# Kernel tuning notes

Hardware: AMD Instinct MI355X
Metric: run time of the kernel (lower is better)

## Reference

```python
import jax, jax.numpy as jnp
import numpy as np
import math

B, N, DIM, H, DH, NNULL = 2, 2048, 1024, 16, 64, 2
SCALE = 8.0
LN_EPS = 1e-5


def _alibi_slopes(heads):
    # heads is a power of 2 here (16): slopes = start * start**i
    start = 2.0 ** (-(2.0 ** (-(math.log2(heads) - 3))))
    return np.array([start * (start ** i) for i in range(heads)], dtype=np.float32)


def setup_inputs() -> dict:
    key = jax.random.key(0)
    ks = jax.random.split(key, 6)
    inner = H * DH
    return {
        "x": jax.random.normal(ks[0], (B, N, DIM), dtype=jnp.float32),
        "norm_g": jnp.ones((DIM,), jnp.float32),
        "norm_b": jnp.zeros((DIM,), jnp.float32),
        "Wq": jax.random.normal(ks[1], (DIM, inner), jnp.float32) * 0.02,
        "Wkv": jax.random.normal(ks[2], (DIM, 2 * inner), jnp.float32) * 0.02,
        "q_scale": jnp.ones((DH,), jnp.float32),
        "k_scale": jnp.ones((DH,), jnp.float32),
        "null_kv": jax.random.normal(ks[3], (H, 2 * NNULL, DH), jnp.float32),
        "Wout": jax.random.normal(ks[4], (inner, DIM), jnp.float32) * 0.02,
    }


def _l2norm(t):
    # matches F.normalize: x / max(||x||, 1e-12)
    n = jnp.sqrt(jnp.sum(t * t, axis=-1, keepdims=True))
    return t / jnp.maximum(n, 1e-12)


def reference(x, norm_g, norm_b, Wq, Wkv, q_scale, k_scale, null_kv, Wout):
    b, n, dim = x.shape
    h, dh, nn = H, DH, NNULL
    j = n + nn

    # NOTE: faithful to source -- K/V come from the PRE-norm x (kv_input bound
    # before x = self.norm(x)); only Q uses the LayerNorm'd x.
    mu = jnp.mean(x, axis=-1, keepdims=True)
    var = jnp.mean((x - mu) ** 2, axis=-1, keepdims=True)
    xn = (x - mu) * jax.lax.rsqrt(var + LN_EPS) * norm_g + norm_b

    q = (xn @ Wq).reshape(b, n, h, dh).transpose(0, 2, 1, 3)          # b h n d
    kv = x @ Wkv
    k, v = jnp.split(kv, 2, axis=-1)
    k = k.reshape(b, n, h, dh).transpose(0, 2, 1, 3)                   # b h n d
    v = v.reshape(b, n, h, dh).transpose(0, 2, 1, 3)

    # null kv: (h, 2*nn, dh) -> (h, nn, 2, dh)
    null = null_kv.reshape(h, nn, 2, dh)
    nk = jnp.broadcast_to(null[:, :, 0, :][None], (b, h, nn, dh))
    nv = jnp.broadcast_to(null[:, :, 1, :][None], (b, h, nn, dh))
    k = jnp.concatenate([nk, k], axis=2)                               # b h j d
    v = jnp.concatenate([nv, v], axis=2)

    q = _l2norm(q) * q_scale
    k = _l2norm(k) * k_scale

    sim = jnp.einsum('bhid,bhjd->bhij', q, k) * SCALE                  # b h n j

    # ALiBi bias: rows at positions j-n..j-1, cols 0..j-1
    irow = jnp.arange(j - n, j)
    jcol = jnp.arange(j)
    bias = -jnp.abs(jcol[None, :] - irow[:, None]).astype(sim.dtype)   # (n, j)
    slopes = jnp.asarray(_alibi_slopes(h))[:, None, None]              # (h,1,1)
    sim = sim + slopes * bias

    # causal mask: triu with offset j - n + 1 (null kv always visible)
    causal = jnp.triu(jnp.ones((n, j), dtype=bool), k=j - n + 1)
    neg = jnp.finfo(sim.dtype).max
    sim = jnp.where(causal[None, None], -neg, sim)

    attn = jax.nn.softmax(sim, axis=-1)
    out = jnp.einsum('bhij,bhjd->bhid', attn, v)
    out = out.transpose(0, 2, 1, 3).reshape(b, n, h * dh)
    return out @ Wout
```

## Files before the change

kernel.cpp:

```cpp
#include <hip/hip_runtime.h>
#include <hip/hip_bf16.h>
#include <stdint.h>

#define H_    16
#define N_    2048
#define DIM_  1024
#define DH_   64
#define NN_   2
#define J_    2050
#define JP_   2112
#define B_    2
#define M_    4096
#define NSEG_ 84

#define S8L_  11.541560327111707f
#define LOG2E_ 1.4426950408889634f

typedef unsigned short u16;
typedef unsigned int u32;
typedef short bf16x8 __attribute__((ext_vector_type(8)));
typedef float f32x4 __attribute__((ext_vector_type(4)));

__device__ __forceinline__ u16 f2b(float f) {
  union { float f; unsigned int i; } v; v.f = f;
  unsigned int r = v.i + 0x7fffu + ((v.i >> 16) & 1u);
  return (u16)(r >> 16);
}
__device__ __forceinline__ float lo2f(u32 u) {
  union { u32 i; float f; } v; v.i = u << 16; return v.f;
}
__device__ __forceinline__ float hi2f(u32 u) {
  union { u32 i; float f; } v; v.i = u & 0xffff0000u; return v.f;
}
__device__ __forceinline__ void unp8(const uint4 u, float* d) {
  d[0] = lo2f(u.x); d[1] = hi2f(u.x); d[2] = lo2f(u.y); d[3] = hi2f(u.y);
  d[4] = lo2f(u.z); d[5] = hi2f(u.z); d[6] = lo2f(u.w); d[7] = hi2f(u.w);
}
__device__ __forceinline__ u32 pk2(float a, float b) {
  union { __hip_bfloat162 h; u32 u; } x;
  x.h = __float22bfloat162_rn(make_float2(a, b));
  return x.u;
}
__device__ __forceinline__ void dma16(const u16* g, u16* l) {
  __builtin_amdgcn_global_load_lds(
      (const __attribute__((address_space(1))) u32*)(const void*)g,
      (__attribute__((address_space(3))) u32*)(void*)l, 16, 0, 0);
}

__global__ __launch_bounds__(256) void prep_k(const float* __restrict__ x,
                                              const float* __restrict__ g,
                                              const float* __restrict__ bb,
                                              const float* __restrict__ Wq,
                                              const float* __restrict__ Wkv,
                                              const float* __restrict__ Wout,
                                              const float* __restrict__ nkv,
                                              const float* __restrict__ ks,
                                              u16* __restrict__ xn,
                                              u16* __restrict__ xbf,
                                              u16* __restrict__ WqT,
                                              u16* __restrict__ WkvT,
                                              u16* __restrict__ WoutT,
                                              u16* __restrict__ Kb,
                                              u16* __restrict__ VTp) {
  __shared__ float tile[32][33];
  __shared__ float red[8];
  int bx = blockIdx.x, by = blockIdx.y;
  int t = threadIdx.x;
  if (bx < 128) {
    const float* in; u16* out; int C; int cx;
    if (bx < 32)      { in = Wq;   out = WqT;   C = 1024; cx = bx; }
    else if (bx < 96) { in = Wkv;  out = WkvT;  C = 2048; cx = bx - 32; }
    else              { in = Wout; out = WoutT; C = 1024; cx = bx - 96; }
    const int R = 1024;
    int tx = t & 31, ty = t >> 5;
    int c0 = cx * 32, r0 = by * 32;
    #pragma unroll
    for (int i = 0; i < 32; i += 8)
      tile[ty + i][tx] = in[(size_t)(r0 + ty + i) * C + c0 + tx];
    __syncthreads();
    #pragma unroll
    for (int i = 0; i < 32; i += 8)
      out[(size_t)(c0 + ty + i) * R + r0 + tx] = f2b(tile[tx][ty + i]);
  } else if (bx < 256) {
    int row = (bx - 128) * 32 + by;
    float4 rw = *(const float4*)(x + (size_t)row * DIM_ + t * 4);
    float v0 = rw.x, v1 = rw.y, v2 = rw.z, v3 = rw.w;
    uint2 cw;
    cw.x = pk2(v0, v1);
    cw.y = pk2(v2, v3);
    *(uint2*)(xbf + (size_t)row * DIM_ + t * 4) = cw;
    float s = v0 + v1 + v2 + v3;
    float ss = v0 * v0 + v1 * v1 + v2 * v2 + v3 * v3;
    #pragma unroll
    for (int o = 32; o; o >>= 1) { s += __shfl_xor(s, o, 64); ss += __shfl_xor(ss, o, 64); }
    int lane = t & 63, w = t >> 6;
    if (lane == 0) { red[w] = s; red[4 + w] = ss; }
    __syncthreads();
    float S = red[0] + red[1] + red[2] + red[3];
    float SS = red[4] + red[5] + red[6] + red[7];
    float mu = S * (1.0f / DIM_);
    float var = SS * (1.0f / DIM_) - mu * mu;
    float rs = rsqrtf(var + 1e-5f);
    float4 gv = *(const float4*)(g + t * 4);
    float4 bv = *(const float4*)(bb + t * 4);
    uint2 ow;
    ow.x = pk2((v0 - mu) * rs * gv.x + bv.x, (v1 - mu) * rs * gv.y + bv.y);
    ow.y = pk2((v2 - mu) * rs * gv.z + bv.z, (v3 - mu) * rs * gv.w + bv.w);
    *(uint2*)(xn + (size_t)row * DIM_ + t * 4) = ow;
  } else if (bx == 256) {
    int bh = by, h = bh & 15;
    if (t < 128) {
      int j = t >> 6, d = t & 63;
      float kv = nkv[(size_t)(h * 4 + 2 * j) * 64 + d];
      float vv = nkv[(size_t)(h * 4 + 2 * j + 1) * 64 + d];
      float ssp = kv * kv;
      #pragma unroll
      for (int o = 32; o; o >>= 1) ssp += __shfl_xor(ssp, o, 64);
      float inv = 1.0f / fmaxf(sqrtf(ssp), 1e-12f);
      Kb[((size_t)bh * JP_ + j) * 64 + d] = f2b(kv * inv * ks[d]);
      VTp[((size_t)bh * 64 + d) * JP_ + j] = f2b(vv);
    }
  } else if (bx == 257) {
    int bh = by;
    uint4 z = {0, 0, 0, 0};
    u16* dst = Kb + ((size_t)bh * JP_ + 2048) * 64 + t * 16;
    ((uint4*)dst)[0] = z;
    ((uint4*)dst)[1] = z;
  } else {
    int bh = by;
    uint4 z = {0, 0, 0, 0};
    int d = t >> 2, p0 = (t & 3) * 16;
    u16* dst = VTp + ((size_t)bh * 64 + d) * JP_ + 2048 + p0;
    ((uint4*)dst)[0] = z;
    ((uint4*)dst)[1] = z;
  }
}

template <int MODE>
__global__ __launch_bounds__(256) void gemm_k(const u16* __restrict__ A,
                                              const u16* __restrict__ BT,
                                              void* __restrict__ dst0,
                                              void* __restrict__ dst1,
                                              const float* __restrict__ scale,
                                              int M, int Nc, int K) {
  __shared__ u16 As[2][128 * 64];
  __shared__ u16 Bs[2][128 * 64];
  int tid = threadIdx.x, wv = tid >> 6, lane = tid & 63;
  int fm = lane & 15, fg = lane >> 4;
  int fg4 = fg * 4;
  int wr = wv >> 1, wc = wv & 1;
  int nlin = (int)blockIdx.x + (int)gridDim.x * (int)blockIdx.y;
  int gx = (int)gridDim.x;
  int ypc = (int)gridDim.y >> 3;
  int mm = nlin >> 3;
  int row0 = ((nlin & 7) * ypc + mm / gx) * 128;
  int col0 = (mm % gx) * 128;
  f32x4 acc[4][4] = {};
  int srow = lane >> 3;
  int skb = ((lane & 7) ^ srow) * 8;
  const u16* Ag = A + (size_t)(row0 + wv * 32 + srow) * K + skb;
  const u16* Bg = BT + (size_t)(col0 + wv * 32 + srow) * K + skb;
  int fr7 = fm & 7;
  int ak0 = (fg ^ fr7) * 8;
  int ak1 = ((fg + 4) ^ fr7) * 8;
  auto stageg = [&](int k0, int buf) {
    u16* AsW = As[buf] + (wv * 32) * 64;
    u16* BsW = Bs[buf] + (wv * 32) * 64;
    dma16(Ag + k0,                    AsW);
    dma16(Ag + (size_t)8 * K + k0,    AsW + 8 * 64);
    dma16(Ag + (size_t)16 * K + k0,   AsW + 16 * 64);
    dma16(Ag + (size_t)24 * K + k0,   AsW + 24 * 64);
    dma16(Bg + k0,                    BsW);
    dma16(Bg + (size_t)8 * K + k0,    BsW + 8 * 64);
    dma16(Bg + (size_t)16 * K + k0,   BsW + 16 * 64);
    dma16(Bg + (size_t)24 * K + k0,   BsW + 24 * 64);
  };
  stageg(0, 0);
  __syncthreads();
  int cur = 0;
  for (int k0 = 0; k0 < K; k0 += 64) {
    if (k0 + 64 < K) stageg(k0 + 64, cur ^ 1);
    bf16x8 af0[4], af1[4], bf0[4], bf1[4];
    #pragma unroll
    for (int mt = 0; mt < 4; mt++) {
      int rbase = (wr * 64 + mt * 16 + fm) * 64;
      af0[mt] = *(const bf16x8*)&As[cur][rbase + ak0];
      af1[mt] = *(const bf16x8*)&As[cur][rbase + ak1];
    }
    #pragma unroll
    for (int nt = 0; nt < 4; nt++) {
      int rbase = (wc * 64 + nt * 16 + fm) * 64;
      bf0[nt] = *(const bf16x8*)&Bs[cur][rbase + ak0];
      bf1[nt] = *(const bf16x8*)&Bs[cur][rbase + ak1];
    }
    #pragma unroll
    for (int mt = 0; mt < 4; mt++)
      #pragma unroll
      for (int nt = 0; nt < 4; nt++) {
        acc[mt][nt] = __builtin_amdgcn_mfma_f32_16x16x32_bf16(af0[mt], bf0[nt], acc[mt][nt], 0, 0, 0);
        acc[mt][nt] = __builtin_amdgcn_mfma_f32_16x16x32_bf16(af1[mt], bf1[nt], acc[mt][nt], 0, 0, 0);
      }
    __syncthreads();
    cur ^= 1;
  }
  int colw = col0 + wc * 64;
  if (MODE == 1) {
    float* C = (float*)dst0;
    #pragma unroll
    for (int mt = 0; mt < 4; mt++)
      #pragma unroll
      for (int r = 0; r < 4; r++) {
        int m = row0 + wr * 64 + mt * 16 + fg4 + r;
        #pragma unroll
        for (int nt = 0; nt < 4; nt++)
          C[(size_t)m * Nc + colw + nt * 16 + fm] = acc[mt][nt][r];
      }
  } else {
    bool isK = (MODE == 2) || (colw < 1024);
    int h = (isK ? colw : colw - 1024) >> 6;
    if (isK) {
      float sv[4];
      #pragma unroll
      for (int nt = 0; nt < 4; nt++) sv[nt] = scale[nt * 16 + fm];
      if (MODE == 2) {
        #pragma unroll
        for (int nt = 0; nt < 4; nt++) sv[nt] *= S8L_;
      }
      u16* Do = (u16*)dst0;
      #pragma unroll
      for (int mt = 0; mt < 4; mt++) {
        #pragma unroll
        for (int r = 0; r < 4; r++) {
          float ssp = 0.0f;
          #pragma unroll
          for (int nt = 0; nt < 4; nt++) ssp += acc[mt][nt][r] * acc[mt][nt][r];
          #pragma unroll
          for (int o = 1; o <= 8; o <<= 1) ssp += __shfl_xor(ssp, o, 64);
          float inv = 1.0f / fmaxf(sqrtf(ssp), 1e-12f);
          int m = row0 + wr * 64 + mt * 16 + fg4 + r;
          int b = m >> 11, n = m & 2047;
          size_t base;
          if (MODE == 2) base = (((size_t)(b * H_ + h)) * N_ + n) * 64;
          else           base = (((size_t)(b * H_ + h)) * JP_ + (n + NN_)) * 64;
          #pragma unroll
          for (int nt = 0; nt < 4; nt++)
            Do[base + nt * 16 + fm] = f2b(acc[mt][nt][r] * inv * sv[nt]);
        }
      }
    } else {
      u16* Do = (u16*)dst1;
      #pragma unroll
      for (int mt = 0; mt < 4; mt++) {
        #pragma unroll
        for (int r = 0; r < 4; r++) {
          int m = row0 + wr * 64 + mt * 16 + fg4 + r;
          int b = m >> 11, n = m & 2047;
          int j = n + NN_;
          int c2 = j >> 6, jl = j & 63;
          int rem = jl & 31;
          int pos = (jl >> 5) * 32 + ((rem >> 2) & 3) * 8 + (rem >> 4) * 4 + (rem & 3);
          size_t hb = (size_t)(b * H_ + h) * 64;
          int off = c2 * 64 + pos;
          #pragma unroll
          for (int nt = 0; nt < 4; nt++)
            Do[(hb + nt * 16 + fm) * JP_ + off] = f2b(acc[mt][nt][r]);
        }
      }
    }
  }
}

__global__ __launch_bounds__(256, 6) void attn_k(const u16* __restrict__ Qn,
                                                 const u16* __restrict__ Kb,
                                                 const u16* __restrict__ VTp,
                                                 const float* __restrict__ qs,
                                                 const float* __restrict__ ks,
                                                 u16* __restrict__ partials) {
  __shared__ u16 Ks0[64 * 32], Ks1[64 * 32];
  __shared__ u16 Vs0[64 * 32], Vs1[64 * 32];
  int tid = threadIdx.x;
  int wv = tid >> 6, lane = tid & 63;
  int fm = lane & 15, fg = lane >> 4;
  int n = (int)blockIdx.x + NSEG_ * (int)blockIdx.y;
  int m = n >> 3;
  int bh = (n & 7) * 4 + m / NSEG_;
  int segid = m % NSEG_;
  int h = bh & 15;
  int cum = 0, qt = 0, seg = 0;
  #pragma unroll 1
  for (int i = 0; i < 32; i++) {
    int t = 31 - i, s = (t + 9) >> 3;
    if (segid < cum + s) { qt = t; seg = segid - cum; break; }
    cum += s;
  }
  int q0 = qt * 64;
  int q = q0 + wv * 16 + fm;
  float slope = exp2f(-0.5f * (float)(h + 1));
  float prod = fabsf(qs[lane] * ks[lane]);
  #pragma unroll
  for (int o = 32; o; o >>= 1) prod = fmaxf(prod, __shfl_xor(prod, o, 64));
  float MbL = 8.0f * prod * LOG2E_;
  float slopeL = slope * LOG2E_;
  const u16* qp = Qn + ((size_t)bh * N_ + q) * 64 + fg * 8;
  bf16x8 qf0 = *(const bf16x8*)(qp);
  bf16x8 qf1 = *(const bf16x8*)(qp + 32);
  f32x4 accO[4] = {};
  float lp = 0.0f;
  int lr = lane >> 2;
  int kbs = ((lane & 3) ^ ((lane >> 3) & 3)) * 8;
  int fs = (fg ^ ((fm >> 1) & 3)) * 8;
  const u16* KbBH = Kb + (size_t)bh * JP_ * 64;
  const u16* VTbh = VTp + (size_t)bh * 64 * JP_;
  int c0 = seg * 8;
  int c1 = min(c0 + 8, qt + 2);
  float bias0 = slopeL * (float)(c0 * 64 + fg * 4 - q - 2) - MbL;
  float sr1 = slopeL, sr2 = slopeL * 2.0f, sr3 = slopeL * 3.0f;
  float s16 = slopeL * 16.0f;
  float d64 = slopeL * 64.0f;
  for (int c = c0; c < c1; c++) {
    int jb = c * 64;
    __syncthreads();
    const u16* Kg = KbBH + (size_t)(jb + wv * 16 + lr) * 64 + kbs;
    dma16(Kg,      Ks0 + wv * 512);
    dma16(Kg + 32, Ks1 + wv * 512);
    const u16* Vg = VTbh + (size_t)(wv * 16 + lr) * JP_ + jb + kbs;
    dma16(Vg,      Vs0 + wv * 512);
    dma16(Vg + 32, Vs1 + wv * 512);
    __syncthreads();
    f32x4 accS[4] = {};
    #pragma unroll
    for (int nt = 0; nt < 4; nt++) {
      bf16x8 kf0 = *(const bf16x8*)&Ks0[(nt * 16 + fm) * 32 + fs];
      accS[nt] = __builtin_amdgcn_mfma_f32_16x16x32_bf16(kf0, qf0, accS[nt], 0, 0, 0);
      bf16x8 kf1 = *(const bf16x8*)&Ks1[(nt * 16 + fm) * 32 + fs];
      accS[nt] = __builtin_amdgcn_mfma_f32_16x16x32_bf16(kf1, qf1, accS[nt], 0, 0, 0);
    }
    union { bf16x8 v; u32 u[4]; } P0, P1;
    float lps = 0.0f;
    float bnt = bias0;
    if (c < qt) {
      #pragma unroll
      for (int nt = 0; nt < 4; nt++) {
        float e0 = __builtin_amdgcn_exp2f(accS[nt][0] + bnt);
        float e1 = __builtin_amdgcn_exp2f((accS[nt][1] + sr1) + bnt);
        float e2 = __builtin_amdgcn_exp2f((accS[nt][2] + sr2) + bnt);
        float e3 = __builtin_amdgcn_exp2f((accS[nt][3] + sr3) + bnt);
        u32 w0 = pk2(e0, e1);
        u32 w1 = pk2(e2, e3);
        lps += (e0 + e1) + (e2 + e3);
        if (nt < 2) { P0.u[nt * 2] = w0; P0.u[nt * 2 + 1] = w1; }
        else        { P1.u[(nt - 2) * 2] = w0; P1.u[(nt - 2) * 2 + 1] = w1; }
        bnt += s16;
      }
    } else {
      int thr = q + 2 - jb;
      #pragma unroll
      for (int nt = 0; nt < 4; nt++) {
        int ib = nt * 16 + fg * 4;
        float e0 = __builtin_amdgcn_exp2f(accS[nt][0] + bnt);
        float e1 = __builtin_amdgcn_exp2f((accS[nt][1] + sr1) + bnt);
        float e2 = __builtin_amdgcn_exp2f((accS[nt][2] + sr2) + bnt);
        float e3 = __builtin_amdgcn_exp2f((accS[nt][3] + sr3) + bnt);
        e0 = (ib + 0 <= thr) ? e0 : 0.0f;
        e1 = (ib + 1 <= thr) ? e1 : 0.0f;
        e2 = (ib + 2 <= thr) ? e2 : 0.0f;
        e3 = (ib + 3 <= thr) ? e3 : 0.0f;
        u32 w0 = pk2(e0, e1);
        u32 w1 = pk2(e2, e3);
        lps += (e0 + e1) + (e2 + e3);
        if (nt < 2) { P0.u[nt * 2] = w0; P0.u[nt * 2 + 1] = w1; }
        else        { P1.u[(nt - 2) * 2] = w0; P1.u[(nt - 2) * 2 + 1] = w1; }
        bnt += s16;
      }
    }
    lp += lps;
    bias0 += d64;
    #pragma unroll
    for (int nt = 0; nt < 4; nt++) {
      bf16x8 vf0 = *(const bf16x8*)&Vs0[(nt * 16 + fm) * 32 + fs];
      accO[nt] = __builtin_amdgcn_mfma_f32_16x16x32_bf16(vf0, P0.v, accO[nt], 0, 0, 0);
      bf16x8 vf1 = *(const bf16x8*)&Vs1[(nt * 16 + fm) * 32 + fs];
      accO[nt] = __builtin_amdgcn_mfma_f32_16x16x32_bf16(vf1, P1.v, accO[nt], 0, 0, 0);
    }
  }
  lp += __shfl_xor(lp, 16, 64);
  lp += __shfl_xor(lp, 32, 64);
  u16* P = partials + ((size_t)bh * NSEG_ + segid) * 4224;
  int sq = wv * 16 + fm;
  #pragma unroll
  for (int nt = 0; nt < 4; nt++) {
    uint2 ow;
    ow.x = pk2(accO[nt][0], accO[nt][1]);
    ow.y = pk2(accO[nt][2], accO[nt][3]);
    *(uint2*)(P + sq * 64 + nt * 16 + fg * 4) = ow;
  }
  if (fg == 0) *(float*)(P + 4096 + 2 * sq) = lp;
}

__global__ __launch_bounds__(256) void comb_k(const u16* __restrict__ partials,
                                              u16* __restrict__ AO) {
  int qt = blockIdx.x, bh = blockIdx.y, b = bh >> 4, h = bh & 15;
  int t = threadIdx.x, q = t >> 2, dq = (t & 3) * 16;
  int s = (qt + 9) >> 3;
  int cum = 0;
  for (int tt = qt + 1; tt < 32; tt++) cum += (tt + 9) >> 3;
  float acc[16] = {};
  float lsum = 0.0f;
  for (int k = 0; k < s; k++) {
    const u16* P = partials + ((size_t)bh * NSEG_ + cum + k) * 4224;
    uint4 a = *(const uint4*)(P + q * 64 + dq);
    uint4 bq = *(const uint4*)(P + q * 64 + dq + 8);
    float tmp[8];
    unp8(a, tmp);
    #pragma unroll
    for (int e = 0; e < 8; e++) acc[e] += tmp[e];
    unp8(bq, tmp);
    #pragma unroll
    for (int e = 0; e < 8; e++) acc[8 + e] += tmp[e];
    lsum += *(const float*)(P + 4096 + 2 * q);
  }
  float linv = 1.0f / lsum;
  int n = qt * 64 + q;
  u16* dst = AO + (((size_t)(b * N_ + n)) * H_ + h) * 64 + dq;
  u16 ov[16] __attribute__((aligned(16)));
  #pragma unroll
  for (int e = 0; e < 16; e++) ov[e] = f2b(acc[e] * linv);
  *(uint4*)dst = ((uint4*)ov)[0];
  *(uint4*)(dst + 8) = ((uint4*)ov)[1];
}

extern "C" void kernel_launch(void* const* d_in, const int* in_sizes, int n_in,
                              void* d_out, int out_size, void* d_ws, size_t ws_size,
                              hipStream_t stream) {
  const float* x    = (const float*)d_in[0];
  const float* ng   = (const float*)d_in[1];
  const float* nb   = (const float*)d_in[2];
  const float* Wq   = (const float*)d_in[3];
  const float* Wkv  = (const float*)d_in[4];
  const float* qs   = (const float*)d_in[5];
  const float* ks   = (const float*)d_in[6];
  const float* nkv  = (const float*)d_in[7];
  const float* Wout = (const float*)d_in[8];
  float* out = (float*)d_out;
  char* ws = (char*)d_ws;

  u16* xn    = (u16*)(ws + 0);
  u16* WoutT = (u16*)(ws + 8388608);
  u16* Qn    = (u16*)(ws + 10485760);
  u16* Kb    = (u16*)(ws + 18874368);
  u16* VTp   = (u16*)(ws + 27525120);
  u16* xbf   = (u16*)(ws + 36175872);
  u16* WqT   = (u16*)(ws + 44564480);
  u16* WkvT  = (u16*)(ws + 46661632);
  u16* parts = xbf;
  u16* AO    = xn;

  prep_k<<<dim3(259, 32), 256, 0, stream>>>(x, ng, nb, Wq, Wkv, Wout, nkv, ks,
                                            xn, xbf, WqT, WkvT, WoutT, Kb, VTp);
  gemm_k<2><<<dim3(8, 32), 256, 0, stream>>>(xn, WqT, Qn, nullptr, qs, M_, 1024, 1024);
  gemm_k<3><<<dim3(16, 32), 256, 0, stream>>>(xbf, WkvT, Kb, VTp, ks, M_, 2048, 1024);
  attn_k<<<dim3(NSEG_, 32), 256, 0, stream>>>(Qn, Kb, VTp, qs, ks, parts);
  comb_k<<<dim3(32, 32), 256, 0, stream>>>(parts, AO);
  gemm_k<1><<<dim3(8, 32), 256, 0, stream>>>(AO, WoutT, out, nullptr, nullptr, M_, 1024, 1024);
}
```

Measured before the change: 211.5 us.

## Merge Q and KV projection GEMMs into one launch and double-buffer K in attention

The Q and KV projection GEMMs now run as a single 768-block launch that branches on block index, removing one kernel launch and the tail between the two GEMMs. In the attention kernel, K tiles are double-buffered: the next K tile is prefetched while the current one is used, and explicit vmcnt waits with split barriers replace the two full __syncthreads per iteration. This is meant to hide K load latency behind compute. In exchange, the attention kernel uses more LDS, and the prefetch on the last iteration reads one K tile past c1, which relies on the padded buffer staying in bounds.

```diff
diff --git a/kernel.cpp b/kernel.cpp
--- a/kernel.cpp
+++ b/kernel.cpp
@@ -136,24 +136,31 @@
   }
 }
 
-template <int MODE>
-__global__ __launch_bounds__(256) void gemm_k(const u16* __restrict__ A,
-                                              const u16* __restrict__ BT,
-                                              void* __restrict__ dst0,
-                                              void* __restrict__ dst1,
-                                              const float* __restrict__ scale,
-                                              int M, int Nc, int K) {
+__global__ __launch_bounds__(256) void gemmqkv_k(const u16* __restrict__ xn,
+                                                 const u16* __restrict__ WqT,
+                                                 const u16* __restrict__ xbf,
+                                                 const u16* __restrict__ WkvT,
+                                                 u16* __restrict__ Qn,
+                                                 u16* __restrict__ Kb,
+                                                 u16* __restrict__ VTp,
+                                                 const float* __restrict__ qs,
+                                                 const float* __restrict__ ks) {
   __shared__ u16 As[2][128 * 64];
   __shared__ u16 Bs[2][128 * 64];
+  const int K = 1024;
   int tid = threadIdx.x, wv = tid >> 6, lane = tid & 63;
   int fm = lane & 15, fg = lane >> 4;
   int fg4 = fg * 4;
   int wr = wv >> 1, wc = wv & 1;
-  int nlin = (int)blockIdx.x + (int)gridDim.x * (int)blockIdx.y;
-  int gx = (int)gridDim.x;
-  int ypc = (int)gridDim.y >> 3;
-  int mm = nlin >> 3;
-  int row0 = ((nlin & 7) * ypc + mm / gx) * 128;
+  int nlin = (int)blockIdx.x;
+  bool isQ = nlin < 256;
+  const u16* A;
+  const u16* BT;
+  int gx, local;
+  if (isQ) { A = xn;  BT = WqT;  gx = 8;  local = nlin; }
+  else     { A = xbf; BT = WkvT; gx = 16; local = nlin - 256; }
+  int mm = local >> 3;
+  int row0 = ((local & 7) * 4 + mm / gx) * 128;
   int col0 = (mm % gx) * 128;
   f32x4 acc[4][4] = {};
   int srow = lane >> 3;
@@ -204,70 +211,132 @@
     cur ^= 1;
   }
   int colw = col0 + wc * 64;
-  if (MODE == 1) {
-    float* C = (float*)dst0;
-    #pragma unroll
-    for (int mt = 0; mt < 4; mt++)
+  bool isK = isQ || (colw < 1024);
+  int h = (isK ? colw : colw - 1024) >> 6;
+  if (isK) {
+    const float* scale = isQ ? qs : ks;
+    float sv[4];
+    #pragma unroll
+    for (int nt = 0; nt < 4; nt++) sv[nt] = scale[nt * 16 + fm];
+    if (isQ) {
+      #pragma unroll
+      for (int nt = 0; nt < 4; nt++) sv[nt] *= S8L_;
+    }
+    u16* Do = isQ ? Qn : Kb;
+    #pragma unroll
+    for (int mt = 0; mt < 4; mt++) {
+      #pragma unroll
+      for (int r = 0; r < 4; r++) {
+        float ssp = 0.0f;
+        #pragma unroll
+        for (int nt = 0; nt < 4; nt++) ssp += acc[mt][nt][r] * acc[mt][nt][r];
+        #pragma unroll
+        for (int o = 1; o <= 8; o <<= 1) ssp += __shfl_xor(ssp, o, 64);
+        float inv = 1.0f / fmaxf(sqrtf(ssp), 1e-12f);
+        int m = row0 + wr * 64 + mt * 16 + fg4 + r;
+        int b = m >> 11, n = m & 2047;
+        size_t base;
+        if (isQ) base = (((size_t)(b * H_ + h)) * N_ + n) * 64;
+        else     base = (((size_t)(b * H_ + h)) * JP_ + (n + NN_)) * 64;
+        #pragma unroll
+        for (int nt = 0; nt < 4; nt++)
+          Do[base + nt * 16 + fm] = f2b(acc[mt][nt][r] * inv * sv[nt]);
+      }
+    }
+  } else {
+    #pragma unroll
+    for (int mt = 0; mt < 4; mt++) {
       #pragma unroll
       for (int r = 0; r < 4; r++) {
         int m = row0 + wr * 64 + mt * 16 + fg4 + r;
+        int b = m >> 11, n = m & 2047;
+        int j = n + NN_;
+        int c2 = j >> 6, jl = j & 63;
+        int rem = jl & 31;
+        int pos = (jl >> 5) * 32 + ((rem >> 2) & 3) * 8 + (rem >> 4) * 4 + (rem & 3);
+        size_t hb = (size_t)(b * H_ + h) * 64;
+        int off = c2 * 64 + pos;
         #pragma unroll
         for (int nt = 0; nt < 4; nt++)
-          C[(size_t)m * Nc + colw + nt * 16 + fm] = acc[mt][nt][r];
+          VTp[(hb + nt * 16 + fm) * JP_ + off] = f2b(acc[mt][nt][r]);
       }
-  } else {
-    bool isK = (MODE == 2) || (colw < 1024);
-    int h = (isK ? colw : colw - 1024) >> 6;
-    if (isK) {
-      float sv[4];
-      #pragma unroll
-      for (int nt = 0; nt < 4; nt++) sv[nt] = scale[nt * 16 + fm];
-      if (MODE == 2) {
-        #pragma unroll
-        for (int nt = 0; nt < 4; nt++) sv[nt] *= S8L_;
+    }
+  }
+}
+
+__global__ __launch_bounds__(256) void gemm1_k(const u16* __restrict__ A,
+                                               const u16* __restrict__ BT,
+                                               float* __restrict__ C,
+                                               int M, int Nc, int K) {
+  __shared__ u16 As[2][128 * 64];
+  __shared__ u16 Bs[2][128 * 64];
+  int tid = threadIdx.x, wv = tid >> 6, lane = tid & 63;
+  int fm = lane & 15, fg = lane >> 4;
+  int fg4 = fg * 4;
+  int wr = wv >> 1, wc = wv & 1;
+  int nlin = (int)blockIdx.x + (int)gridDim.x * (int)blockIdx.y;
+  int gx = (int)gridDim.x;
+  int mm = nlin >> 3;
+  int row0 = ((nlin & 7) * 4 + mm / gx) * 128;
+  int col0 = (mm % gx) * 128;
+  f32x4 acc[4][4] = {};
+  int srow = lane >> 3;
+  int skb = ((lane & 7) ^ srow) * 8;
+  const u16* Ag = A + (size_t)(row0 + wv * 32 + srow) * K + skb;
+  const u16* Bg = BT + (size_t)(col0 + wv * 32 + srow) * K + skb;
+  int fr7 = fm & 7;
+  int ak0 = (fg ^ fr7) * 8;
+  int ak1 = ((fg + 4) ^ fr7) * 8;
+  auto stageg = [&](int k0, int buf) {
+    u16* AsW = As[buf] + (wv * 32) * 64;
+    u16* BsW = Bs[buf] + (wv * 32) * 64;
+    dma16(Ag + k0,                    AsW);
+    dma16(Ag + (size_t)8 * K + k0,    AsW + 8 * 64);
+    dma16(Ag + (size_t)16 * K + k0,   AsW + 16 * 64);
+    dma16(Ag + (size_t)24 * K + k0,   AsW + 24 * 64);
+    dma16(Bg + k0,                    BsW);
+    dma16(Bg + (size_t)8 * K + k0,    BsW + 8 * 64);
+    dma16(Bg + (size_t)16 * K + k0,   BsW + 16 * 64);
+    dma16(Bg + (size_t)24 * K + k0,   BsW + 24 * 64);
+  };
+  stageg(0, 0);
+  __syncthreads();
+  int cur = 0;
+  for (int k0 = 0; k0 < K; k0 += 64) {
+    if (k0 + 64 < K) stageg(k0 + 64, cur ^ 1);
+    bf16x8 af0[4], af1[4], bf0[4], bf1[4];
+    #pragma unroll
+    for (int mt = 0; mt < 4; mt++) {
+      int rbase = (wr * 64 + mt * 16 + fm) * 64;
+      af0[mt] = *(const bf16x8*)&As[cur][rbase + ak0];
+      af1[mt] = *(const bf16x8*)&As[cur][rbase + ak1];
+    }
+    #pragma unroll
+    for (int nt = 0; nt < 4; nt++) {
+      int rbase = (wc * 64 + nt * 16 + fm) * 64;
+      bf0[nt] = *(const bf16x8*)&Bs[cur][rbase + ak0];
+      bf1[nt] = *(const bf16x8*)&Bs[cur][rbase + ak1];
+    }
+    #pragma unroll
+    for (int mt = 0; mt < 4; mt++)
+      #pragma unroll
+      for (int nt = 0; nt < 4; nt++) {
+        acc[mt][nt] = __builtin_amdgcn_mfma_f32_16x16x32_bf16(af0[mt], bf0[nt], acc[mt][nt], 0, 0, 0);
+        acc[mt][nt] = __builtin_amdgcn_mfma_f32_16x16x32_bf16(af1[mt], bf1[nt], acc[mt][nt], 0, 0, 0);
       }
-      u16* Do = (u16*)dst0;
-      #pragma unroll
-      for (int mt = 0; mt < 4; mt++) {
-        #pragma unroll
-        for (int r = 0; r < 4; r++) {
-          float ssp = 0.0f;
-          #pragma unroll
-          for (int nt = 0; nt < 4; nt++) ssp += acc[mt][nt][r] * acc[mt][nt][r];
-          #pragma unroll
-          for (int o = 1; o <= 8; o <<= 1) ssp += __shfl_xor(ssp, o, 64);
-          float inv = 1.0f / fmaxf(sqrtf(ssp), 1e-12f);
-          int m = row0 + wr * 64 + mt * 16 + fg4 + r;
-          int b = m >> 11, n = m & 2047;
-          size_t base;
-          if (MODE == 2) base = (((size_t)(b * H_ + h)) * N_ + n) * 64;
-          else           base = (((size_t)(b * H_ + h)) * JP_ + (n + NN_)) * 64;
-          #pragma unroll
-          for (int nt = 0; nt < 4; nt++)
-            Do[base + nt * 16 + fm] = f2b(acc[mt][nt][r] * inv * sv[nt]);
-        }
-      }
-    } else {
-      u16* Do = (u16*)dst1;
-      #pragma unroll
-      for (int mt = 0; mt < 4; mt++) {
-        #pragma unroll
-        for (int r = 0; r < 4; r++) {
-          int m = row0 + wr * 64 + mt * 16 + fg4 + r;
-          int b = m >> 11, n = m & 2047;
-          int j = n + NN_;
-          int c2 = j >> 6, jl = j & 63;
-          int rem = jl & 31;
-          int pos = (jl >> 5) * 32 + ((rem >> 2) & 3) * 8 + (rem >> 4) * 4 + (rem & 3);
-          size_t hb = (size_t)(b * H_ + h) * 64;
-          int off = c2 * 64 + pos;
-          #pragma unroll
-          for (int nt = 0; nt < 4; nt++)
-            Do[(hb + nt * 16 + fm) * JP_ + off] = f2b(acc[mt][nt][r]);
-        }
-      }
-    }
-  }
+    __syncthreads();
+    cur ^= 1;
+  }
+  int colw = col0 + wc * 64;
+  #pragma unroll
+  for (int mt = 0; mt < 4; mt++)
+    #pragma unroll
+    for (int r = 0; r < 4; r++) {
+      int m = row0 + wr * 64 + mt * 16 + fg4 + r;
+      #pragma unroll
+      for (int nt = 0; nt < 4; nt++)
+        C[(size_t)m * Nc + colw + nt * 16 + fm] = acc[mt][nt][r];
+    }
 }
 
 __global__ __launch_bounds__(256, 6) void attn_k(const u16* __restrict__ Qn,
@@ -276,7 +345,7 @@
                                                  const float* __restrict__ qs,
                                                  const float* __restrict__ ks,
                                                  u16* __restrict__ partials) {
-  __shared__ u16 Ks0[64 * 32], Ks1[64 * 32];
+  __shared__ u16 Ks0[2][64 * 32], Ks1[2][64 * 32];
   __shared__ u16 Vs0[64 * 32], Vs1[64 * 32];
   int tid = threadIdx.x;
   int wv = tid >> 6, lane = tid & 63;
@@ -317,22 +386,33 @@
   float sr1 = slopeL, sr2 = slopeL * 2.0f, sr3 = slopeL * 3.0f;
   float s16 = slopeL * 16.0f;
   float d64 = slopeL * 64.0f;
+  {
+    const u16* Kg = KbBH + (size_t)(c0 * 64 + wv * 16 + lr) * 64 + kbs;
+    dma16(Kg,      Ks0[0] + wv * 512);
+    dma16(Kg + 32, Ks1[0] + wv * 512);
+  }
+  asm volatile("s_waitcnt vmcnt(2)" ::: "memory");
+  __builtin_amdgcn_sched_barrier(0);
+  int cur = 0;
+  #pragma unroll 1
   for (int c = c0; c < c1; c++) {
     int jb = c * 64;
-    __syncthreads();
-    const u16* Kg = KbBH + (size_t)(jb + wv * 16 + lr) * 64 + kbs;
-    dma16(Kg,      Ks0 + wv * 512);
-    dma16(Kg + 32, Ks1 + wv * 512);
     const u16* Vg = VTbh + (size_t)(wv * 16 + lr) * JP_ + jb + kbs;
     dma16(Vg,      Vs0 + wv * 512);
     dma16(Vg + 32, Vs1 + wv * 512);
-    __syncthreads();
+    const u16* Kg = KbBH + (size_t)(jb + 64 + wv * 16 + lr) * 64 + kbs;
+    dma16(Kg,      Ks0[cur ^ 1] + wv * 512);
+    dma16(Kg + 32, Ks1[cur ^ 1] + wv * 512);
+    asm volatile("s_waitcnt vmcnt(4)" ::: "memory");
+    __builtin_amdgcn_sched_barrier(0);
+    __builtin_amdgcn_s_barrier();
+    __builtin_amdgcn_sched_barrier(0);
     f32x4 accS[4] = {};
     #pragma unroll
     for (int nt = 0; nt < 4; nt++) {
-      bf16x8 kf0 = *(const bf16x8*)&Ks0[(nt * 16 + fm) * 32 + fs];
+      bf16x8 kf0 = *(const bf16x8*)&Ks0[cur][(nt * 16 + fm) * 32 + fs];
       accS[nt] = __builtin_amdgcn_mfma_f32_16x16x32_bf16(kf0, qf0, accS[nt], 0, 0, 0);
-      bf16x8 kf1 = *(const bf16x8*)&Ks1[(nt * 16 + fm) * 32 + fs];
+      bf16x8 kf1 = *(const bf16x8*)&Ks1[cur][(nt * 16 + fm) * 32 + fs];
       accS[nt] = __builtin_amdgcn_mfma_f32_16x16x32_bf16(kf1, qf1, accS[nt], 0, 0, 0);
     }
     union { bf16x8 v; u32 u[4]; } P0, P1;
@@ -375,6 +455,10 @@
     }
     lp += lps;
     bias0 += d64;
+    asm volatile("s_waitcnt vmcnt(2)" ::: "memory");
+    __builtin_amdgcn_sched_barrier(0);
+    __builtin_amdgcn_s_barrier();
+    __builtin_amdgcn_sched_barrier(0);
     #pragma unroll
     for (int nt = 0; nt < 4; nt++) {
       bf16x8 vf0 = *(const bf16x8*)&Vs0[(nt * 16 + fm) * 32 + fs];
@@ -382,6 +466,11 @@
       bf16x8 vf1 = *(const bf16x8*)&Vs1[(nt * 16 + fm) * 32 + fs];
       accO[nt] = __builtin_amdgcn_mfma_f32_16x16x32_bf16(vf1, P1.v, accO[nt], 0, 0, 0);
     }
+    asm volatile("s_waitcnt lgkmcnt(0)" ::: "memory");
+    __builtin_amdgcn_sched_barrier(0);
+    __builtin_amdgcn_s_barrier();
+    __builtin_amdgcn_sched_barrier(0);
+    cur ^= 1;
   }
   lp += __shfl_xor(lp, 16, 64);
   lp += __shfl_xor(lp, 32, 64);
@@ -457,9 +546,8 @@
 
   prep_k<<<dim3(259, 32), 256, 0, stream>>>(x, ng, nb, Wq, Wkv, Wout, nkv, ks,
                                             xn, xbf, WqT, WkvT, WoutT, Kb, VTp);
-  gemm_k<2><<<dim3(8, 32), 256, 0, stream>>>(xn, WqT, Qn, nullptr, qs, M_, 1024, 1024);
-  gemm_k<3><<<dim3(16, 32), 256, 0, stream>>>(xbf, WkvT, Kb, VTp, ks, M_, 2048, 1024);
+  gemmqkv_k<<<768, 256, 0, stream>>>(xn, WqT, xbf, WkvT, Qn, Kb, VTp, qs, ks);
   attn_k<<<dim3(NSEG_, 32), 256, 0, stream>>>(Qn, Kb, VTp, qs, ks, parts);
   comb_k<<<dim3(32, 32), 256, 0, stream>>>(parts, AO);
-  gemm_k<1><<<dim3(8, 32), 256, 0, stream>>>(AO, WoutT, out, nullptr, nullptr, M_, 1024, 1024);
-}
+  gemm1_k<<<dim3(8, 32), 256, 0, stream>>>(AO, WoutT, out, M_, 1024, 1024);
+}
```

New measurement: 214.7 us. Within noise of the previous version (+1.5%).
